# Kernel optimization log

Hardware: AMD Instinct MI355X
Metric: run time of the kernel (lower is better)

The kernel has to match this reference:

```python
import jax, jax.numpy as jnp
import numpy as np

N_NODES = 100000
BN_EPS = 1e-5


def _cheb_bn_prelu(x, src, dst, w, W, b, a, g, be):
    # ChebConv K=3 with sym normalization, lambda_max=2 => L_hat = -D^-1/2 A D^-1/2
    def lap(v):
        return jax.ops.segment_sum(w[:, None] * v[src], dst, num_segments=N_NODES)
    Tx1 = lap(x)                      # [N, F]
    Tx2 = 2.0 * lap(Tx1) - x
    out = x @ W[0] + Tx1 @ W[1] + Tx2 @ W[2] + b
    out = jnp.where(out > 0, out, a * out)          # PReLU (single param)
    mu = out.mean(0)
    var = out.var(0)                                 # biased, as torch BN
    return (out - mu) / jnp.sqrt(var + BN_EPS) * g + be


def setup_inputs() -> dict:
    key = jax.random.key(0)
    ks = jax.random.split(key, 40)
    N, E, H = N_NODES, 3200000, 64
    inp = {
        'x': jax.random.normal(ks[0], (N, 3), jnp.float32),
        'pos': jax.random.normal(ks[1], (N, 3), jnp.float32),
        'normals': jax.random.normal(ks[2], (N, 3), jnp.float32),
        'edge_index': jax.random.randint(ks[3], (2, E), 0, N, jnp.int64 if jax.config.read('jax_enable_x64') else jnp.int32),
    }
    dims = [(9, H), (H, H), (H, H), (H, H // 2)]
    i = 4
    for m, (fi, fo) in enumerate(dims, start=1):
        s = 1.0 / np.sqrt(fi)
        inp[f'W{m}'] = jax.random.uniform(ks[i], (3, fi, fo), jnp.float32, -s, s); i += 1
        inp[f'b{m}'] = jax.random.uniform(ks[i], (fo,), jnp.float32, -s, s); i += 1
        inp[f'a{m}'] = jnp.full((1,), 0.25, jnp.float32)
        inp[f'g{m}'] = jnp.ones((fo,), jnp.float32)
        inp[f'be{m}'] = jnp.zeros((fo,), jnp.float32)
    hh = H // 2
    for m in range(1, 4):
        s = 1.0 / np.sqrt(hh)
        inp[f'h{m}w'] = jax.random.uniform(ks[i], (hh, hh), jnp.float32, -s, s); i += 1
        inp[f'h{m}b'] = jax.random.uniform(ks[i], (hh,), jnp.float32, -s, s); i += 1
    return inp


def reference(x, pos, normals, edge_index,
              W1, b1, a1, g1, be1, W2, b2, a2, g2, be2,
              W3, b3, a3, g3, be3, W4, b4, a4, g4, be4,
              h1w, h1b, h2w, h2b, h3w, h3b):
    src, dst = edge_index[0], edge_index[1]
    deg = jax.ops.segment_sum(jnp.ones(src.shape[0], x.dtype), src, num_segments=N_NODES)
    dis = jnp.where(deg > 0, jax.lax.rsqrt(jnp.maximum(deg, 1.0)), 0.0)
    w = -dis[src] * dis[dst]                         # scaled Laplacian edge weights
    h = jnp.concatenate([x, pos, normals], axis=1)   # [N, 9]
    h = _cheb_bn_prelu(h, src, dst, w, W1, b1, a1, g1, be1)
    h = _cheb_bn_prelu(h, src, dst, w, W2, b2, a2, g2, be2)
    h = _cheb_bn_prelu(h, src, dst, w, W3, b3, a3, g3, be3)
    h = _cheb_bn_prelu(h, src, dst, w, W4, b4, a4, g4, be4)
    h = jax.nn.relu(h @ h1w + h1b)
    h = jax.nn.relu(h @ h2w + h2b)
    return h @ h3w + h3b                              # [N, 32] logits
```

## Files before the change

kernel.cpp:

```cpp
#include <hip/hip_runtime.h>

constexpr float BN_EPS = 1e-5f;
constexpr int HB = 256;

__device__ __forceinline__ float bf2f(unsigned short u) {
  return __uint_as_float(((unsigned)u) << 16);
}
__device__ __forceinline__ unsigned short f2bf(float f) {
  union { float f; unsigned u; } v; v.f = f;
  unsigned r = v.u + 0x7FFF + ((v.u >> 16) & 1);
  return (unsigned short)(r >> 16);
}


__global__ void __launch_bounds__(1024) hist_lds_kernel(const int* __restrict__ keys, int E, int slice,
                                                        unsigned* __restrict__ partials, int NW) {
  extern __shared__ unsigned lds[];
  int tid = threadIdx.x, b = blockIdx.x;
  for (int w = tid; w < NW; w += 1024) lds[w] = 0;
  __syncthreads();
  int e0 = b * slice, e1 = e0 + slice; if (e1 > E) e1 = E;
  for (int e = e0 + tid; e < e1; e += 1024) {
    int n = keys[e];
    atomicAdd(&lds[n >> 2], 1u << (8 * (n & 3)));
  }
  __syncthreads();
  unsigned* out = partials + (size_t)b * NW;
  for (int w = tid; w < NW; w += 1024) out[w] = lds[w];
}

__global__ void combine_kernel(unsigned* __restrict__ pA, const unsigned* __restrict__ pB,
                               float* __restrict__ dis, int* __restrict__ cnt, int NW, int N) {
  int w = blockIdx.x * blockDim.x + threadIdx.x;
  if (w >= NW) return;
  unsigned sumA = 0;
  for (int b = 0; b < HB; ++b) sumA += pA[(size_t)b * NW + w];
  unsigned runB = 0;
  for (int b = 0; b < HB; ++b) {
    unsigned v = pB[(size_t)b * NW + w];
    pA[(size_t)b * NW + w] = runB;
    runB += v;
  }
  int n0 = w * 4;
#pragma unroll
  for (int j = 0; j < 4; ++j) {
    int n = n0 + j;
    if (n < N) {
      unsigned da = (sumA >> (8 * j)) & 255u;
      unsigned db = (runB >> (8 * j)) & 255u;
      dis[n] = da > 0 ? rsqrtf((float)da) : 0.f;
      cnt[n] = (int)db;
    }
  }
}

__global__ void scan1_kernel(const int* __restrict__ cnt, int N,
                             int* __restrict__ rowptr, int* __restrict__ bsums) {
  int tid = threadIdx.x, lane = tid & 63, wid = tid >> 6;
  int i = blockIdx.x * 256 + tid;
  int v = (i < N) ? cnt[i] : 0;
  int incl = v;
#pragma unroll
  for (int off = 1; off < 64; off <<= 1) {
    int u = __shfl_up(incl, off);
    if (lane >= off) incl += u;
  }
  __shared__ int wt[4];
  if (lane == 63) wt[wid] = incl;
  __syncthreads();
  int woff = 0;
  for (int w = 0; w < wid; ++w) woff += wt[w];
  if (i < N) rowptr[i] = woff + incl - v;
  if (tid == 255) bsums[blockIdx.x] = woff + incl;
}

__global__ void scan2_kernel(int* __restrict__ bsums, int NB, int* __restrict__ rowptr, int N) {
  int tid = threadIdx.x, lane = tid & 63, wid = tid >> 6;
  int v = (tid < NB) ? bsums[tid] : 0;
  int incl = v;
#pragma unroll
  for (int off = 1; off < 64; off <<= 1) {
    int u = __shfl_up(incl, off);
    if (lane >= off) incl += u;
  }
  __shared__ int wt[16];
  if (lane == 63) wt[wid] = incl;
  __syncthreads();
  int woff = 0;
  for (int w = 0; w < wid; ++w) woff += wt[w];
  if (tid < NB) bsums[tid] = woff + incl - v;
  if (tid == blockDim.x - 1) rowptr[N] = woff + incl;
}

__global__ void scan3_kernel(int* __restrict__ rowptr, const int* __restrict__ bsums, int N) {
  int i = blockIdx.x * 256 + threadIdx.x;
  if (i < N) rowptr[i] += bsums[blockIdx.x];
}

__global__ void __launch_bounds__(1024) scatter2_kernel(
    const int* __restrict__ src, const int* __restrict__ dst, int E, int slice,
    const unsigned* __restrict__ baseTbl, int NW, const int* __restrict__ rowptr,
    const float* __restrict__ dis, int2* __restrict__ pk) {
  extern __shared__ unsigned lds[];
  int tid = threadIdx.x, b = blockIdx.x;
  const unsigned* base = baseTbl + (size_t)b * NW;
  for (int w = tid; w < NW; w += 1024) lds[w] = base[w];
  __syncthreads();
  int e0 = b * slice, e1 = e0 + slice; if (e1 > E) e1 = E;
  for (int e = e0 + tid; e < e1; e += 1024) {
    int s = src[e], d = dst[e];
    unsigned prev = atomicAdd(&lds[d >> 2], 1u << (8 * (d & 3)));
    int p = rowptr[d] + (int)((prev >> (8 * (d & 3))) & 255u);
    pk[p] = make_int2(s, __float_as_int(-dis[s] * dis[d]));
  }
}

__global__ void pack_kernel(const float* __restrict__ x, const float* __restrict__ pos,
                            const float* __restrict__ nrm, ushort* __restrict__ h0b, int N) {
  int idx = blockIdx.x * blockDim.x + threadIdx.x;
  if (idx < N * 16) {
    int n = idx >> 4, c = idx & 15;
    float v = 0.f;
    if (c < 3) v = x[n * 3 + c];
    else if (c < 6) v = pos[n * 3 + c - 3];
    else if (c < 9) v = nrm[n * 3 + c - 6];
    h0b[idx] = f2bf(v);
  }
}


template <bool AFFINE>
__global__ __launch_bounds__(256) void lap64_kernel(
    const ushort4* __restrict__ vb, ushort4* __restrict__ outb,
    const int* __restrict__ rowptr, const int2* __restrict__ pk,
    const float* __restrict__ st, int N) {
  int tid = threadIdx.x, lane = tid & 63, wid = tid >> 6;
  int node = blockIdx.x * 4 + wid;
  if (node >= N) return;
  int g = lane >> 4, q = lane & 15;
  int r0 = rowptr[node], r1 = rowptr[node + 1];
  float4 a = {0.f, 0.f, 0.f, 0.f}, b = {0.f, 0.f, 0.f, 0.f};
  float ws = 0.f, ws2 = 0.f;
  int k = r0 + g;
  for (; k + 12 < r1; k += 16) {
    int2 p0 = pk[k], p1 = pk[k + 4], p2 = pk[k + 8], p3 = pk[k + 12];
    ushort4 u0 = vb[(size_t)p0.x * 16 + q];
    ushort4 u1 = vb[(size_t)p1.x * 16 + q];
    ushort4 u2 = vb[(size_t)p2.x * 16 + q];
    ushort4 u3 = vb[(size_t)p3.x * 16 + q];
    float w0 = __int_as_float(p0.y), w1 = __int_as_float(p1.y);
    float w2 = __int_as_float(p2.y), w3 = __int_as_float(p3.y);
    ws += w0 + w2; ws2 += w1 + w3;
    a.x = fmaf(w0, bf2f(u0.x), a.x); a.y = fmaf(w0, bf2f(u0.y), a.y);
    a.z = fmaf(w0, bf2f(u0.z), a.z); a.w = fmaf(w0, bf2f(u0.w), a.w);
    b.x = fmaf(w1, bf2f(u1.x), b.x); b.y = fmaf(w1, bf2f(u1.y), b.y);
    b.z = fmaf(w1, bf2f(u1.z), b.z); b.w = fmaf(w1, bf2f(u1.w), b.w);
    a.x = fmaf(w2, bf2f(u2.x), a.x); a.y = fmaf(w2, bf2f(u2.y), a.y);
    a.z = fmaf(w2, bf2f(u2.z), a.z); a.w = fmaf(w2, bf2f(u2.w), a.w);
    b.x = fmaf(w3, bf2f(u3.x), b.x); b.y = fmaf(w3, bf2f(u3.y), b.y);
    b.z = fmaf(w3, bf2f(u3.z), b.z); b.w = fmaf(w3, bf2f(u3.w), b.w);
  }
  for (; k < r1; k += 4) {
    int2 p0 = pk[k];
    ushort4 u0 = vb[(size_t)p0.x * 16 + q];
    float w0 = __int_as_float(p0.y);
    ws += w0;
    a.x = fmaf(w0, bf2f(u0.x), a.x); a.y = fmaf(w0, bf2f(u0.y), a.y);
    a.z = fmaf(w0, bf2f(u0.z), a.z); a.w = fmaf(w0, bf2f(u0.w), a.w);
  }
  a.x += b.x; a.y += b.y; a.z += b.z; a.w += b.w; ws += ws2;
  a.x += __shfl_xor(a.x, 16); a.y += __shfl_xor(a.y, 16);
  a.z += __shfl_xor(a.z, 16); a.w += __shfl_xor(a.w, 16);
  ws += __shfl_xor(ws, 16);
  a.x += __shfl_xor(a.x, 32); a.y += __shfl_xor(a.y, 32);
  a.z += __shfl_xor(a.z, 32); a.w += __shfl_xor(a.w, 32);
  ws += __shfl_xor(ws, 32);
  if (g == 0) {
    float4 o = a;
    if (AFFINE) {
      float4 s4 = *(const float4*)(st + q * 4);
      float4 t4 = *(const float4*)(st + 64 + q * 4);
      o.x = fmaf(a.x, s4.x, ws * t4.x);
      o.y = fmaf(a.y, s4.y, ws * t4.y);
      o.z = fmaf(a.z, s4.z, ws * t4.z);
      o.w = fmaf(a.w, s4.w, ws * t4.w);
    }
    ushort4 ub;
    ub.x = f2bf(o.x); ub.y = f2bf(o.y); ub.z = f2bf(o.z); ub.w = f2bf(o.w);
    outb[(size_t)node * 16 + q] = ub;
  }
}


__global__ __launch_bounds__(256) void lap16_kernel(const ushort4* __restrict__ vb,
                                                    ushort4* __restrict__ outb,
                                                    const int* __restrict__ rowptr,
                                                    const int2* __restrict__ pk, int N) {
  int tid = threadIdx.x, lane = tid & 63, wid = tid >> 6;
  int node = (blockIdx.x * 4 + wid) * 4 + (lane >> 4);
  int sub = lane & 15, g = sub >> 2, q = sub & 3;
  float4 acc = {0.f, 0.f, 0.f, 0.f};
  if (node < N) {
    int r0 = rowptr[node], r1 = rowptr[node + 1];
    for (int k = r0 + g; k < r1; k += 4) {
      int2 pr = pk[k];
      float w = __int_as_float(pr.y);
      ushort4 u = vb[(size_t)pr.x * 4 + q];
      acc.x = fmaf(w, bf2f(u.x), acc.x); acc.y = fmaf(w, bf2f(u.y), acc.y);
      acc.z = fmaf(w, bf2f(u.z), acc.z); acc.w = fmaf(w, bf2f(u.w), acc.w);
    }
  }
  acc.x += __shfl_xor(acc.x, 4); acc.y += __shfl_xor(acc.y, 4);
  acc.z += __shfl_xor(acc.z, 4); acc.w += __shfl_xor(acc.w, 4);
  acc.x += __shfl_xor(acc.x, 8); acc.y += __shfl_xor(acc.y, 8);
  acc.z += __shfl_xor(acc.z, 8); acc.w += __shfl_xor(acc.w, 8);
  if (node < N && g == 0) {
    ushort4 ub;
    ub.x = f2bf(acc.x); ub.y = f2bf(acc.y); ub.z = f2bf(acc.z); ub.w = f2bf(acc.w);
    outb[(size_t)node * 4 + q] = ub;
  }
}


template <int F_IN, int F_OUT, bool NORMH>
__global__ __launch_bounds__(256) void mm_kernel(
    const ushort* hb, const ushort* t1b, const ushort* t2b,
    ushort* outb,
    const float* __restrict__ W, const float* __restrict__ bias,
    const float* __restrict__ aP, const float* __restrict__ stPrev,
    float* __restrict__ bp, int N, int f_in_real, int ntiles) {
  constexpr int CPT = F_OUT / 16;
  constexpr int WSZ = 3 * F_IN * F_OUT;
  constexpr int RSZ = 16 * F_OUT * 2;
  constexpr int SM = (WSZ > RSZ) ? WSZ : RSZ;
  __shared__ float sm[SM];
  __shared__ float smS[F_IN], smT[F_IN];

  int tid = threadIdx.x;
  const int S = f_in_real * F_OUT;
  for (int idx = tid; idx < WSZ; idx += 256) {
    int m = idx / (F_IN * F_OUT);
    int r = idx - m * (F_IN * F_OUT);
    int i = r / F_OUT, c = r - i * F_OUT;
    float v = 0.f;
    if (i < f_in_real) {
      int b = i * F_OUT + c;
      if (m == 0)      v = W[b] - W[2 * S + b];
      else if (m == 1) v = W[S + b];
      else             v = 2.f * W[2 * S + b];
    }
    sm[idx] = v;
  }
  if (NORMH && tid < F_IN) { smS[tid] = stPrev[tid]; smT[tid] = stPrev[64 + tid]; }
  __syncthreads();

  const int cg = tid & 15;
  const int ngt = tid >> 4;
  const int c0 = cg * CPT;
  const float alpha = aP[0];
  float bb[CPT];
#pragma unroll
  for (int c = 0; c < CPT; ++c) bb[c] = bias[c0 + c];

  float ssum[CPT], ssq[CPT];
#pragma unroll
  for (int c = 0; c < CPT; ++c) { ssum[c] = 0.f; ssq[c] = 0.f; }

  for (int tile = blockIdx.x; tile < ntiles; tile += gridDim.x) {
    const int node0 = tile * 64 + ngt * 4;
    float acc[4][CPT];
#pragma unroll
    for (int j = 0; j < 4; ++j)
#pragma unroll
      for (int c = 0; c < CPT; ++c) acc[j][c] = 0.f;

#pragma unroll
    for (int m = 0; m < 3; ++m) {
      const ushort* A = (m == 0 ? hb : (m == 1 ? t1b : t2b)) + (size_t)node0 * F_IN;
      const float* Bm = sm + m * F_IN * F_OUT;
#pragma unroll 2
      for (int kb = 0; kb < F_IN / 4; ++kb) {
        float ar[4][4];
#pragma unroll
        for (int j = 0; j < 4; ++j) {
          ushort4 u = *(const ushort4*)(A + j * F_IN + kb * 4);
          ar[j][0] = bf2f(u.x); ar[j][1] = bf2f(u.y);
          ar[j][2] = bf2f(u.z); ar[j][3] = bf2f(u.w);
        }
        if (NORMH && m == 0) {
          float4 sv = *(const float4*)(smS + kb * 4);
          float4 tv = *(const float4*)(smT + kb * 4);
#pragma unroll
          for (int j = 0; j < 4; ++j) {
            ar[j][0] = fmaf(ar[j][0], sv.x, tv.x);
            ar[j][1] = fmaf(ar[j][1], sv.y, tv.y);
            ar[j][2] = fmaf(ar[j][2], sv.z, tv.z);
            ar[j][3] = fmaf(ar[j][3], sv.w, tv.w);
          }
        }
#pragma unroll
        for (int kk = 0; kk < 4; ++kk) {
          const float* Brow = Bm + (kb * 4 + kk) * F_OUT + c0;
          float br[CPT];
          if constexpr (CPT == 4) *(float4*)br = *(const float4*)Brow;
          else                    *(float2*)br = *(const float2*)Brow;
#pragma unroll
          for (int j = 0; j < 4; ++j)
#pragma unroll
            for (int c = 0; c < CPT; ++c)
              acc[j][c] = fmaf(ar[j][kk], br[c], acc[j][c]);
        }
      }
    }

#pragma unroll
    for (int j = 0; j < 4; ++j) {
      int node = node0 + j;
      if (node < N) {
        float v[CPT];
#pragma unroll
        for (int c = 0; c < CPT; ++c) {
          float t = acc[j][c] + bb[c];
          t = t > 0.f ? t : alpha * t;
          v[c] = t;
          ssum[c] += t;
          ssq[c] += t * t;
        }
        ushort* o = outb + (size_t)node * 64 + c0;
        if constexpr (CPT == 4) {
          uint2 ub;
          ub.x = (unsigned)f2bf(v[0]) | ((unsigned)f2bf(v[1]) << 16);
          ub.y = (unsigned)f2bf(v[2]) | ((unsigned)f2bf(v[3]) << 16);
          *(uint2*)o = ub;
        } else {
          unsigned ub = (unsigned)f2bf(v[0]) | ((unsigned)f2bf(v[1]) << 16);
          *(unsigned*)o = ub;
        }
      }
    }
  }

  __syncthreads();
#pragma unroll
  for (int c = 0; c < CPT; ++c) {
    sm[(ngt * F_OUT + c0 + c) * 2 + 0] = ssum[c];
    sm[(ngt * F_OUT + c0 + c) * 2 + 1] = ssq[c];
  }
  __syncthreads();
  if (tid < 128) {
    int col = tid & 63, stat = tid >> 6;
    float tot = 0.f;
    if (col < F_OUT) {
#pragma unroll 8
      for (int g = 0; g < 16; ++g) tot += sm[(g * F_OUT + col) * 2 + stat];
    }
    bp[(size_t)blockIdx.x * 128 + stat * 64 + col] = tot;
  }
}


__global__ void stats_kernel(const float* __restrict__ bp, int nb,
                             const float* __restrict__ g, const float* __restrict__ be,
                             float* __restrict__ st, int F_OUT, float invN) {
  __shared__ float red[1024];
  int tid = threadIdx.x;
  int t = tid & 127, c = tid >> 7;
  float s = 0.f;
  for (int w = c; w < nb; w += 8) s += bp[(size_t)w * 128 + t];
  red[tid] = s;
  __syncthreads();
  if (tid < 128) {
    float tot = 0.f;
    for (int cc = 0; cc < 8; ++cc) tot += red[cc * 128 + tid];
    red[tid] = tot;
  }
  __syncthreads();
  if (tid < F_OUT) {
    float sum = red[tid], sq = red[64 + tid];
    float mu = sum * invN;
    float var = sq * invN - mu * mu;
    float sc = g[tid] * rsqrtf(var + BN_EPS);
    st[tid] = sc;
    st[64 + tid] = be[tid] - mu * sc;
  }
}


__global__ __launch_bounds__(256) void mlp_kernel(const ushort* __restrict__ hb,
    const float* __restrict__ st,
    const float* __restrict__ w1, const float* __restrict__ b1,
    const float* __restrict__ w2, const float* __restrict__ b2,
    const float* __restrict__ w3, const float* __restrict__ b3,
    float* __restrict__ out, int N) {
  __shared__ float W1[1024], W2[1024], W3[1024], B1[32], B2[32], B3[32], S4[32], T4[32];
  int tid = threadIdx.x;
  for (int idx = tid; idx < 1024; idx += 256) {
    W1[idx] = w1[idx];
    W2[idx] = w2[idx];
    W3[idx] = w3[idx];
  }
  if (tid < 32) {
    B1[tid] = b1[tid]; B2[tid] = b2[tid]; B3[tid] = b3[tid];
    S4[tid] = st[tid]; T4[tid] = st[64 + tid];
  }
  __syncthreads();
  int j = tid & 31;
  int n = blockIdx.x * 8 + (tid >> 5);
  if (n >= N) return;
  float v = fmaf(bf2f(hb[(size_t)n * 64 + j]), S4[j], T4[j]);
  float a1 = B1[j];
#pragma unroll
  for (int i = 0; i < 32; ++i) a1 += __shfl(v, i, 32) * W1[i * 32 + j];
  a1 = fmaxf(a1, 0.f);
  float a2 = B2[j];
#pragma unroll
  for (int i = 0; i < 32; ++i) a2 += __shfl(a1, i, 32) * W2[i * 32 + j];
  a2 = fmaxf(a2, 0.f);
  float a3 = B3[j];
#pragma unroll
  for (int i = 0; i < 32; ++i) a3 += __shfl(a2, i, 32) * W3[i * 32 + j];
  out[(size_t)n * 32 + j] = a3;
}


extern "C" void kernel_launch(void* const* d_in, const int* in_sizes, int n_in,
                              void* d_out, int out_size, void* d_ws, size_t ws_size,
                              hipStream_t stream) {
  const float* x   = (const float*)d_in[0];
  const float* pos = (const float*)d_in[1];
  const float* nrm = (const float*)d_in[2];
  const int*   ei  = (const int*)d_in[3];
  const float* W1p = (const float*)d_in[4];
  const float* b1p = (const float*)d_in[5];
  const float* a1p = (const float*)d_in[6];
  const float* g1p = (const float*)d_in[7];
  const float* be1p= (const float*)d_in[8];
  const float* W2p = (const float*)d_in[9];
  const float* b2p = (const float*)d_in[10];
  const float* a2p = (const float*)d_in[11];
  const float* g2p = (const float*)d_in[12];
  const float* be2p= (const float*)d_in[13];
  const float* W3p = (const float*)d_in[14];
  const float* b3p = (const float*)d_in[15];
  const float* a3p = (const float*)d_in[16];
  const float* g3p = (const float*)d_in[17];
  const float* be3p= (const float*)d_in[18];
  const float* W4p = (const float*)d_in[19];
  const float* b4p = (const float*)d_in[20];
  const float* a4p = (const float*)d_in[21];
  const float* g4p = (const float*)d_in[22];
  const float* be4p= (const float*)d_in[23];
  const float* h1w = (const float*)d_in[24];
  const float* h1b = (const float*)d_in[25];
  const float* h2w = (const float*)d_in[26];
  const float* h2b = (const float*)d_in[27];
  const float* h3w = (const float*)d_in[28];
  const float* h3b = (const float*)d_in[29];

  const int N = in_sizes[0] / 3;
  const int E = in_sizes[3] / 2;
  const int* src = ei;
  const int* dst = ei + E;

  const int NW = (N + 3) / 4;
  const size_t ldsBytes = (size_t)NW * 4;
  const int slice = (E + HB - 1) / HB;

  char* p = (char*)d_ws;
  auto alloc = [&](size_t bytes) -> void* {
    void* r = (void*)p;
    p += (bytes + 255) & ~(size_t)255;
    return r;
  };
  float*    dis      = (float*)   alloc((size_t)N * 4);
  int*      rowptr   = (int*)     alloc((size_t)(N + 1) * 4);
  int*      cnt      = (int*)     alloc((size_t)N * 4);
  int*      bsums    = (int*)     alloc(4096 * 4);
  unsigned* partialsA= (unsigned*)alloc((size_t)HB * NW * 4);
  unsigned* partialsB= (unsigned*)alloc((size_t)HB * NW * 4);
  int2*     pk       = (int2*)partialsB;
  ushort*   bufHb    = (ushort*)  alloc((size_t)N * 64 * 2);
  ushort*   bufT1b   = (ushort*)  alloc((size_t)N * 64 * 2);
  ushort*   bufT2b   = (ushort*)  alloc((size_t)N * 64 * 2);
  ushort*   bufH16b  = (ushort*)  alloc((size_t)N * 16 * 2);
  ushort*   bufT116b = (ushort*)  alloc((size_t)N * 16 * 2);
  ushort*   bufT216b = (ushort*)  alloc((size_t)N * 16 * 2);
  const int MMB = 768;
  float*    bp       = (float*)   alloc((size_t)MMB * 128 * 4);
  float*    stats    = (float*)   alloc(512 * 4);
  float* st1 = stats, *st2 = stats + 128, *st3 = stats + 256, *st4 = stats + 384;

  int gN = (N + 255) / 256;
  hist_lds_kernel<<<HB, 1024, ldsBytes, stream>>>(src, E, slice, partialsA, NW);
  hist_lds_kernel<<<HB, 1024, ldsBytes, stream>>>(dst, E, slice, partialsB, NW);
  combine_kernel<<<(NW + 255) / 256, 256, 0, stream>>>(partialsA, partialsB, dis, cnt, NW, N);
  scan1_kernel<<<gN, 256, 0, stream>>>(cnt, N, rowptr, bsums);
  scan2_kernel<<<1, 1024, 0, stream>>>(bsums, gN, rowptr, N);
  scan3_kernel<<<gN, 256, 0, stream>>>(rowptr, bsums, N);
  scatter2_kernel<<<HB, 1024, ldsBytes, stream>>>(src, dst, E, slice, partialsA, NW, rowptr, dis, pk);
  pack_kernel<<<(N * 16 + 255) / 256, 256, 0, stream>>>(x, pos, nrm, bufH16b, N);

  const float invN = 1.f / (float)N;
  int g64 = (N + 3) / 4, g16 = (N + 15) / 16;
  const int ntiles = (N + 63) / 64;

  lap16_kernel<<<g16, 256, 0, stream>>>((const ushort4*)bufH16b, (ushort4*)bufT116b, rowptr, pk, N);
  lap16_kernel<<<g16, 256, 0, stream>>>((const ushort4*)bufT116b, (ushort4*)bufT216b, rowptr, pk, N);
  mm_kernel<16, 64, false><<<MMB, 256, 0, stream>>>(bufH16b, bufT116b, bufT216b, bufHb,
      W1p, b1p, a1p, nullptr, bp, N, 9, ntiles);
  stats_kernel<<<1, 1024, 0, stream>>>(bp, MMB, g1p, be1p, st1, 64, invN);

  lap64_kernel<true><<<g64, 256, 0, stream>>>((const ushort4*)bufHb, (ushort4*)bufT1b,
      rowptr, pk, st1, N);
  lap64_kernel<false><<<g64, 256, 0, stream>>>((const ushort4*)bufT1b, (ushort4*)bufT2b,
      rowptr, pk, nullptr, N);
  mm_kernel<64, 64, true><<<MMB, 256, 0, stream>>>(bufHb, bufT1b, bufT2b, bufHb,
      W2p, b2p, a2p, st1, bp, N, 64, ntiles);
  stats_kernel<<<1, 1024, 0, stream>>>(bp, MMB, g2p, be2p, st2, 64, invN);

  lap64_kernel<true><<<g64, 256, 0, stream>>>((const ushort4*)bufHb, (ushort4*)bufT1b,
      rowptr, pk, st2, N);
  lap64_kernel<false><<<g64, 256, 0, stream>>>((const ushort4*)bufT1b, (ushort4*)bufT2b,
      rowptr, pk, nullptr, N);
  mm_kernel<64, 64, true><<<MMB, 256, 0, stream>>>(bufHb, bufT1b, bufT2b, bufHb,
      W3p, b3p, a3p, st2, bp, N, 64, ntiles);
  stats_kernel<<<1, 1024, 0, stream>>>(bp, MMB, g3p, be3p, st3, 64, invN);

  lap64_kernel<true><<<g64, 256, 0, stream>>>((const ushort4*)bufHb, (ushort4*)bufT1b,
      rowptr, pk, st3, N);
  lap64_kernel<false><<<g64, 256, 0, stream>>>((const ushort4*)bufT1b, (ushort4*)bufT2b,
      rowptr, pk, nullptr, N);
  mm_kernel<64, 32, true><<<MMB, 256, 0, stream>>>(bufHb, bufT1b, bufT2b, bufHb,
      W4p, b4p, a4p, st3, bp, N, 64, ntiles);
  stats_kernel<<<1, 1024, 0, stream>>>(bp, MMB, g4p, be4p, st4, 32, invN);

  mlp_kernel<<<(N + 7) / 8, 256, 0, stream>>>(bufHb, st4, h1w, h1b, h2w, h2b, h3w, h3b,
      (float*)d_out, N);
}
```

Measured before the change: 941.4 us.

## Register-tile the final MLP with LDS activations and a persistent grid

Rewrites the three-layer head MLP so each thread computes a 4-node by 4-column register tile per layer. Intermediate activations are staged in LDS, replacing the per-node wavefront shuffles. The kernel now loops persistently over 128-node tiles with a fixed grid of 768 blocks instead of one block per 8 nodes, which cuts weight reloads into LDS and shuffle overhead. The cost is more LDS use per block, extra barriers per tile, and uncoalesced 8-byte reads of the bf16 input rows.

Result: faster. 908.4 us (-3.5%).

```diff
diff --git a/kernel.cpp b/kernel.cpp
--- a/kernel.cpp
+++ b/kernel.cpp
@@ -391,35 +391,134 @@
     const float* __restrict__ w1, const float* __restrict__ b1,
     const float* __restrict__ w2, const float* __restrict__ b2,
     const float* __restrict__ w3, const float* __restrict__ b3,
-    float* __restrict__ out, int N) {
-  __shared__ float W1[1024], W2[1024], W3[1024], B1[32], B2[32], B3[32], S4[32], T4[32];
+    float* __restrict__ out, int N, int ntiles) {
+  __shared__ float Wl[3][1024];
+  __shared__ float Bl[3][32];
+  __shared__ float S4[32], T4[32];
+  __shared__ float act[2][128][36];
   int tid = threadIdx.x;
   for (int idx = tid; idx < 1024; idx += 256) {
-    W1[idx] = w1[idx];
-    W2[idx] = w2[idx];
-    W3[idx] = w3[idx];
+    Wl[0][idx] = w1[idx];
+    Wl[1][idx] = w2[idx];
+    Wl[2][idx] = w3[idx];
   }
   if (tid < 32) {
-    B1[tid] = b1[tid]; B2[tid] = b2[tid]; B3[tid] = b3[tid];
+    Bl[0][tid] = b1[tid]; Bl[1][tid] = b2[tid]; Bl[2][tid] = b3[tid];
     S4[tid] = st[tid]; T4[tid] = st[64 + tid];
   }
   __syncthreads();
-  int j = tid & 31;
-  int n = blockIdx.x * 8 + (tid >> 5);
-  if (n >= N) return;
-  float v = fmaf(bf2f(hb[(size_t)n * 64 + j]), S4[j], T4[j]);
-  float a1 = B1[j];
-#pragma unroll
-  for (int i = 0; i < 32; ++i) a1 += __shfl(v, i, 32) * W1[i * 32 + j];
-  a1 = fmaxf(a1, 0.f);
-  float a2 = B2[j];
-#pragma unroll
-  for (int i = 0; i < 32; ++i) a2 += __shfl(a1, i, 32) * W2[i * 32 + j];
-  a2 = fmaxf(a2, 0.f);
-  float a3 = B3[j];
-#pragma unroll
-  for (int i = 0; i < 32; ++i) a3 += __shfl(a2, i, 32) * W3[i * 32 + j];
-  out[(size_t)n * 32 + j] = a3;
+
+  const int cg = tid & 7, ng = tid >> 3;
+  const int c0 = cg * 4;
+  const int nl = ng * 4;
+
+  for (int tile = blockIdx.x; tile < ntiles; tile += gridDim.x) {
+    const int node0 = tile * 128 + nl;
+    float acc[4][4];
+
+#pragma unroll
+    for (int j = 0; j < 4; ++j)
+#pragma unroll
+      for (int c = 0; c < 4; ++c) acc[j][c] = 0.f;
+#pragma unroll
+    for (int kb = 0; kb < 8; ++kb) {
+      float ar[4][4];
+#pragma unroll
+      for (int j = 0; j < 4; ++j) {
+        int node = node0 + j;
+        if (node < N) {
+          ushort4 u = *(const ushort4*)(hb + (size_t)node * 64 + kb * 4);
+          ar[j][0] = fmaf(bf2f(u.x), S4[kb * 4 + 0], T4[kb * 4 + 0]);
+          ar[j][1] = fmaf(bf2f(u.y), S4[kb * 4 + 1], T4[kb * 4 + 1]);
+          ar[j][2] = fmaf(bf2f(u.z), S4[kb * 4 + 2], T4[kb * 4 + 2]);
+          ar[j][3] = fmaf(bf2f(u.w), S4[kb * 4 + 3], T4[kb * 4 + 3]);
+        } else {
+          ar[j][0] = ar[j][1] = ar[j][2] = ar[j][3] = 0.f;
+        }
+      }
+#pragma unroll
+      for (int kk = 0; kk < 4; ++kk) {
+        float br[4];
+        *(float4*)br = *(const float4*)(&Wl[0][(kb * 4 + kk) * 32 + c0]);
+#pragma unroll
+        for (int j = 0; j < 4; ++j)
+#pragma unroll
+          for (int c = 0; c < 4; ++c)
+            acc[j][c] = fmaf(ar[j][kk], br[c], acc[j][c]);
+      }
+    }
+#pragma unroll
+    for (int j = 0; j < 4; ++j) {
+      float v[4];
+#pragma unroll
+      for (int c = 0; c < 4; ++c) v[c] = fmaxf(acc[j][c] + Bl[0][c0 + c], 0.f);
+      *(float4*)(&act[0][nl + j][c0]) = *(float4*)v;
+    }
+    __syncthreads();
+
+#pragma unroll
+    for (int j = 0; j < 4; ++j)
+#pragma unroll
+      for (int c = 0; c < 4; ++c) acc[j][c] = 0.f;
+#pragma unroll
+    for (int kb = 0; kb < 8; ++kb) {
+      float ar[4][4];
+#pragma unroll
+      for (int j = 0; j < 4; ++j)
+        *(float4*)ar[j] = *(const float4*)(&act[0][nl + j][kb * 4]);
+#pragma unroll
+      for (int kk = 0; kk < 4; ++kk) {
+        float br[4];
+        *(float4*)br = *(const float4*)(&Wl[1][(kb * 4 + kk) * 32 + c0]);
+#pragma unroll
+        for (int j = 0; j < 4; ++j)
+#pragma unroll
+          for (int c = 0; c < 4; ++c)
+            acc[j][c] = fmaf(ar[j][kk], br[c], acc[j][c]);
+      }
+    }
+#pragma unroll
+    for (int j = 0; j < 4; ++j) {
+      float v[4];
+#pragma unroll
+      for (int c = 0; c < 4; ++c) v[c] = fmaxf(acc[j][c] + Bl[1][c0 + c], 0.f);
+      *(float4*)(&act[1][nl + j][c0]) = *(float4*)v;
+    }
+    __syncthreads();
+
+#pragma unroll
+    for (int j = 0; j < 4; ++j)
+#pragma unroll
+      for (int c = 0; c < 4; ++c) acc[j][c] = 0.f;
+#pragma unroll
+    for (int kb = 0; kb < 8; ++kb) {
+      float ar[4][4];
+#pragma unroll
+      for (int j = 0; j < 4; ++j)
+        *(float4*)ar[j] = *(const float4*)(&act[1][nl + j][kb * 4]);
+#pragma unroll
+      for (int kk = 0; kk < 4; ++kk) {
+        float br[4];
+        *(float4*)br = *(const float4*)(&Wl[2][(kb * 4 + kk) * 32 + c0]);
+#pragma unroll
+        for (int j = 0; j < 4; ++j)
+#pragma unroll
+          for (int c = 0; c < 4; ++c)
+            acc[j][c] = fmaf(ar[j][kk], br[c], acc[j][c]);
+      }
+    }
+#pragma unroll
+    for (int j = 0; j < 4; ++j) {
+      int node = node0 + j;
+      if (node < N) {
+        float v[4];
+#pragma unroll
+        for (int c = 0; c < 4; ++c) v[c] = acc[j][c] + Bl[2][c0 + c];
+        *(float4*)(out + (size_t)node * 32 + c0) = *(float4*)v;
+      }
+    }
+    __syncthreads();
+  }
 }
 
 
@@ -503,6 +602,7 @@
   const float invN = 1.f / (float)N;
   int g64 = (N + 3) / 4, g16 = (N + 15) / 16;
   const int ntiles = (N + 63) / 64;
+  const int ntilesM = (N + 127) / 128;
 
   lap16_kernel<<<g16, 256, 0, stream>>>((const ushort4*)bufH16b, (ushort4*)bufT116b, rowptr, pk, N);
   lap16_kernel<<<g16, 256, 0, stream>>>((const ushort4*)bufT116b, (ushort4*)bufT216b, rowptr, pk, N);
@@ -534,6 +634,6 @@
       W4p, b4p, a4p, st3, bp, N, 64, ntiles);
   stats_kernel<<<1, 1024, 0, stream>>>(bp, MMB, g4p, be4p, st4, 32, invN);
 
-  mlp_kernel<<<(N + 7) / 8, 256, 0, stream>>>(bufHb, st4, h1w, h1b, h2w, h2b, h3w, h3b,
-      (float*)d_out, N);
-}
+  mlp_kernel<<<MMB, 256, 0, stream>>>(bufHb, st4, h1w, h1b, h2w, h2b, h3w, h3b,
+      (float*)d_out, N, ntilesM);
+}
```
